# Optimization experiments

Measured on AMD Instinct MI355X. Metric: run time of the kernel, lower is better.

The kernel has to match this reference:

```python
import jax, jax.numpy as jnp
import numpy as np

C, D, K15, K16, OUT = 64, 8, 15, 16, 512
B = 32768


def setup_inputs() -> dict:
    key = jax.random.key(0)
    kx, kS, kH, kT, kL = jax.random.split(key, 5)
    x = jax.random.normal(kx, (B, C * D), dtype=jnp.float32)
    S = jax.random.normal(kS, (C, D, K15), dtype=jnp.float32)
    H = jax.random.normal(kH, (K15, K16), dtype=jnp.float32)
    T = jax.random.normal(kT, (C, K15), dtype=jnp.float32)
    LUT = jax.random.normal(kL, (C, K16, OUT), dtype=jnp.float32)
    return {"x": x, "S": S, "H": H, "T": T, "LUT": LUT}


def reference(x, S, H, T, LUT):
    b = x.shape[0]
    xv = x.reshape(b, C, D)                              # (B, C, D)
    p = jnp.einsum('bcd,cdk->bck', xv, S) - T            # (B, C, 15)
    # torch sets zeros to -1 before sign => sign(x)==-1 when x<=0
    s = jnp.where(p > 0, jnp.float32(1.0), jnp.float32(-1.0))
    h = jnp.einsum('bck,kj->bcj', s, H)                  # (B, C, 16)
    idx = jnp.argmax(h, axis=-1)                         # (B, C) int
    # one_hot @ LUT == direct gather of LUT[c, idx[b,c], :]
    vals = LUT[jnp.arange(C)[None, :], idx]              # (B, C, OUT)
    return jnp.sum(vals, axis=1)                         # (B, OUT)
```

## Files before the change

### kernel.cpp

```cpp
#include <hip/hip_runtime.h>
#include <stdint.h>

#define B_    32768
#define C_    64
#define D_    8
#define K15_  15
#define K16_  16
#define OUT_  512

typedef _Float16 half4v __attribute__((ext_vector_type(4)));
typedef _Float16 half8  __attribute__((ext_vector_type(8)));

#define AMAP_OFF  0
#define AMAP_SZ   32768
#define S64_OFF   32768
#define S64_SZ    (64 * 15 * 8 * 8)
#define T64_OFF   (S64_OFF + S64_SZ)
#define T64_SZ    (64 * 15 * 8)
#define IDX_OFF   (T64_OFF + T64_SZ)
#define IDX_SZ    (B_ * C_)
#define S32_SZ    (64 * 15 * 8 * 4)
#define PCT_OFF   (IDX_OFF + IDX_SZ)
#define PCT_SZ    (B_ * 32)
#define PTAB_OFF  (PCT_OFF + PCT_SZ)
#define PTAB_SZ   (32 * 32 * 256 * 16 * 2)
#define WS_NEED   ((size_t)PTAB_OFF + PTAB_SZ)

__device__ __forceinline__ void gld_lds16(const void* g, void* l) {
    __builtin_amdgcn_global_load_lds(
        (const __attribute__((address_space(1))) void*)g,
        (__attribute__((address_space(3))) void*)l, 16, 0, 0);
}

__global__ __launch_bounds__(256) void k_setup(const float* __restrict__ LUT,
                                               const float* __restrict__ H,
                                               const float* __restrict__ S,
                                               const float* __restrict__ T,
                                               _Float16* __restrict__ P5,
                                               uint8_t* __restrict__ amap,
                                               double* __restrict__ S64,
                                               double* __restrict__ T64,
                                               float* __restrict__ S32,
                                               float* __restrict__ T32,
                                               int do_pairs) {
    int gid = blockIdx.x * 256 + threadIdx.x;

    if (do_pairs) {
        int e8 = gid & 1;
        int q = (gid >> 1) & 255;
        int jc = (gid >> 9) & 31;
        int p = gid >> 14;
        int t0 = q >> 4;
        int t1 = q & 15;
        int j0 = jc * 16 + e8 * 8;
        const float* u = LUT + (size_t)((2 * p) * 16 + t0) * 512 + j0;
        const float* v = LUT + (size_t)((2 * p + 1) * 16 + t1) * 512 + j0;
        float4 u0 = ((const float4*)u)[0];
        float4 u1 = ((const float4*)u)[1];
        float4 v0 = ((const float4*)v)[0];
        float4 v1 = ((const float4*)v)[1];
        half8 w;
        w[0] = (_Float16)(u0.x + v0.x);
        w[1] = (_Float16)(u0.y + v0.y);
        w[2] = (_Float16)(u0.z + v0.z);
        w[3] = (_Float16)(u0.w + v0.w);
        w[4] = (_Float16)(u1.x + v1.x);
        w[5] = (_Float16)(u1.y + v1.y);
        w[6] = (_Float16)(u1.z + v1.z);
        w[7] = (_Float16)(u1.w + v1.w);
        *(half8*)(P5 + (size_t)gid * 8) = w;
    }

    if (blockIdx.x < 128) {
        int code = gid;
        double h[K16_];
#pragma unroll
        for (int j = 0; j < K16_; ++j) h[j] = 0.0;
#pragma unroll
        for (int k = 0; k < K15_; ++k) {
            double s = ((code >> k) & 1) ? 1.0 : -1.0;
#pragma unroll
            for (int j = 0; j < K16_; ++j) h[j] += s * (double)H[k * K16_ + j];
        }
        double best = h[0];
        int bi = 0;
#pragma unroll
        for (int j = 1; j < K16_; ++j) {
            if (h[j] > best) { best = h[j]; bi = j; }
        }
        amap[code] = (uint8_t)bi;
    } else if (blockIdx.x == 128) {
        for (int i = threadIdx.x; i < 64 * 15 * 8; i += 256) {
            int c = i / 120;
            int r = i - c * 120;
            int k = r >> 3;
            int d = r & 7;
            float sv = S[c * 120 + d * 15 + k];
            S64[i] = (double)sv;
            if (do_pairs) S32[i] = sv;
        }
        for (int i = threadIdx.x; i < 64 * 15; i += 256) {
            T64[i] = (double)T[i];
            if (do_pairs) T32[i] = T[i];
        }
    }
}

#define XSTRIDE 585
template <int FAST>
__global__ __launch_bounds__(256) void k_codes2(const float* __restrict__ x,
                                                const double* __restrict__ S64,
                                                const double* __restrict__ T64,
                                                const float* __restrict__ S32,
                                                const float* __restrict__ T32,
                                                const uint8_t* __restrict__ amap,
                                                uint8_t* __restrict__ idxo,
                                                uint8_t* __restrict__ pcT) {
    __shared__ float xls[32 * XSTRIDE];
    __shared__ uint8_t idsh[64 * 68];

    int b0 = blockIdx.x * 64;
    int lane = threadIdx.x & 63;
    int wv = __builtin_amdgcn_readfirstlane(threadIdx.x >> 6);

    for (int half = 0; half < 2; ++half) {
        __syncthreads();
#pragma unroll
        for (int t = 0; t < 16; ++t) {
            int e = t * 256 + threadIdx.x;
            int b = e >> 6;
            int j4 = e & 63;
            float4 v = ((const float4*)(x + (size_t)(b0 + b) * 512 +
                                        half * 256))[j4];
            int cl = j4 >> 1;
            int d0 = (j4 & 1) * 4;
            float* dst = &xls[cl * XSTRIDE + b * 9 + d0];
            dst[0] = v.x; dst[1] = v.y; dst[2] = v.z; dst[3] = v.w;
        }
        __syncthreads();
        for (int i = 0; i < 8; ++i) {
            int cl = wv + i * 4;
            int c = half * 32 + cl;
            unsigned code = 0;
            if (FAST) {
                const float* Sc = S32 + c * 120;
                const float* Tc = T32 + c * 15;
                float xf[8];
#pragma unroll
                for (int d = 0; d < 8; ++d)
                    xf[d] = xls[cl * XSTRIDE + lane * 9 + d];
                float pmin = 3.0e38f;
#pragma unroll
                for (int k = 0; k < K15_; ++k) {
                    float p = -Tc[k];
#pragma unroll
                    for (int d = 0; d < 8; ++d)
                        p = fmaf(xf[d], Sc[k * 8 + d], p);
                    code |= (p > 0.f) ? (1u << k) : 0u;
                    pmin = fminf(pmin, fabsf(p));
                }
                if (pmin < 1e-4f) {
                    const double* Sd = S64 + c * 120;
                    const double* Td = T64 + c * 15;
                    code = 0;
#pragma unroll
                    for (int k = 0; k < K15_; ++k) {
                        double p = -Td[k];
#pragma unroll
                        for (int d = 0; d < 8; ++d)
                            p = fma((double)xf[d], Sd[k * 8 + d], p);
                        code |= (p > 0.0) ? (1u << k) : 0u;
                    }
                }
            } else {
                const double* Sc = S64 + c * 120;
                const double* Tc = T64 + c * 15;
                double xd[8];
#pragma unroll
                for (int d = 0; d < 8; ++d)
                    xd[d] = (double)xls[cl * XSTRIDE + lane * 9 + d];
#pragma unroll
                for (int k = 0; k < K15_; ++k) {
                    double p = -Tc[k];
#pragma unroll
                    for (int d = 0; d < 8; ++d)
                        p = fma(xd[d], Sc[k * 8 + d], p);
                    code |= (p > 0.0) ? (1u << k) : 0u;
                }
            }
            idsh[lane * 68 + c] = amap[code];
        }
    }
    __syncthreads();

    int bb = threadIdx.x >> 2;
    int q = threadIdx.x & 3;
    if (!FAST) {
        uint32_t w0 = *(const uint32_t*)&idsh[bb * 68 + q * 16 + 0];
        uint32_t w1 = *(const uint32_t*)&idsh[bb * 68 + q * 16 + 4];
        uint32_t w2 = *(const uint32_t*)&idsh[bb * 68 + q * 16 + 8];
        uint32_t w3 = *(const uint32_t*)&idsh[bb * 68 + q * 16 + 12];
        uint32_t* o = (uint32_t*)(idxo + (size_t)(b0 + bb) * 64 + q * 16);
        o[0] = w0; o[1] = w1; o[2] = w2; o[3] = w3;
    }
    {
        int row = b0 + bb;
        int rg = row >> 10;
        int tr = row & 127;
        int i_ = (row & 1023) >> 7;
        uint8_t* base = pcT + rg * 1024 + tr * 8 + i_;
#pragma unroll
        for (int pi = 0; pi < 8; ++pi) {
            int p = q * 8 + pi;
            uint8_t byte = (uint8_t)((idsh[bb * 68 + 2 * p] << 4) |
                                     idsh[bb * 68 + 2 * p + 1]);
            base[p * 32768] = byte;
        }
    }
}

__global__ __launch_bounds__(256, 8) void k_main8(const uint8_t* __restrict__ pcT,
                                                  const _Float16* __restrict__ P5,
                                                  float* __restrict__ out) {
    __shared__ alignas(16) _Float16 slab[2][256 * 16];

    int rg5 = blockIdx.x >> 5;
    int jc = blockIdx.x & 31;
    int t = threadIdx.x;
    int tc = t & 1;
    int tr = t >> 1;
    int lane = t & 63;
    int wv = __builtin_amdgcn_readfirstlane(t >> 6);

    const uint8_t* cbase = pcT + (rg5 >> 1) * 1024 + tr * 8 + (rg5 & 1) * 4;

    float acc[4][8];
#pragma unroll
    for (int i = 0; i < 4; ++i)
#pragma unroll
        for (int e = 0; e < 8; ++e) acc[i][e] = 0.f;

    int hoff = wv * 512 + lane * 8;

    {
        const _Float16* g = P5 + (size_t)jc * 4096 + hoff;
        gld_lds16(g, &slab[0][wv * 512]);
        gld_lds16(g + 2048, &slab[0][wv * 512 + 2048]);
    }
    uint32_t cw = *(const uint32_t*)cbase;
    uint32_t cwn = 0;

    for (int p = 0; p < 32; ++p) {
        __syncthreads();

        if (p < 31) {
            const _Float16* g =
                P5 + (size_t)((p + 1) * 32 + jc) * 4096 + hoff;
            _Float16* d = &slab[(p + 1) & 1][wv * 512];
            gld_lds16(g, d);
            gld_lds16(g + 2048, d + 2048);
            cwn = *(const uint32_t*)(cbase + (size_t)(p + 1) * 32768);
        }

        const _Float16* rb = &slab[p & 1][0] + tc * 8;
        uint32_t cw_cur = cw;
#pragma unroll
        for (int i = 0; i < 4; ++i) {
            int ci = (int)((cw_cur >> (8 * i)) & 0xFF);
            half8 v = *(const half8*)(rb + ci * 16);
#pragma unroll
            for (int e = 0; e < 8; ++e)
                acc[i][e] = fmaf((float)v[e], 1.0f, acc[i][e]);
        }
        cw = cwn;
    }

#pragma unroll
    for (int i = 0; i < 4; ++i) {
        int row = rg5 * 512 + i * 128 + tr;
        float* o = out + (size_t)row * 512 + jc * 16 + tc * 8;
        float4 w0;
        w0.x = acc[i][0]; w0.y = acc[i][1]; w0.z = acc[i][2]; w0.w = acc[i][3];
        float4 w1;
        w1.x = acc[i][4]; w1.y = acc[i][5]; w1.z = acc[i][6]; w1.w = acc[i][7];
        ((float4*)o)[0] = w0;
        ((float4*)o)[1] = w1;
    }
}

__global__ __launch_bounds__(256) void k_main_direct(const uint8_t* __restrict__ idx,
                                                     const float* __restrict__ LUT,
                                                     float* __restrict__ out) {
    int j4 = threadIdx.x & 127;
    int sub = threadIdx.x >> 7;
    int b0 = blockIdx.x * 16 + sub * 8;
    const float4* L4 = (const float4*)LUT;
    for (int r = 0; r < 8; ++r) {
        int b = b0 + r;
        const uint32_t* iw = (const uint32_t*)(idx + (size_t)b * 64);
        float4 acc;
        acc.x = 0.f; acc.y = 0.f; acc.z = 0.f; acc.w = 0.f;
#pragma unroll
        for (int i = 0; i < 16; ++i) {
            uint32_t w = __builtin_amdgcn_readfirstlane(iw[i]);
#pragma unroll
            for (int t = 0; t < 4; ++t) {
                int c = i * 4 + t;
                uint32_t codev = (w >> (8 * t)) & 0xFu;
                float4 v = L4[(size_t)(c * 16 + codev) * 128 + j4];
                acc.x += v.x; acc.y += v.y; acc.z += v.z; acc.w += v.w;
            }
        }
        ((float4*)(out + (size_t)b * 512))[j4] = acc;
    }
}

extern "C" void kernel_launch(void* const* d_in, const int* in_sizes, int n_in,
                              void* d_out, int out_size, void* d_ws, size_t ws_size,
                              hipStream_t stream) {
    const float* x   = (const float*)d_in[0];
    const float* S   = (const float*)d_in[1];
    const float* H   = (const float*)d_in[2];
    const float* T   = (const float*)d_in[3];
    const float* LUT = (const float*)d_in[4];
    float* out = (float*)d_out;

    uint8_t* ws = (uint8_t*)d_ws;
    uint8_t* amap = ws + AMAP_OFF;
    double* S64   = (double*)(ws + S64_OFF);
    double* T64   = (double*)(ws + T64_OFF);
    uint8_t* idxb = ws + IDX_OFF;
    float* S32    = (float*)(ws + IDX_OFF);
    float* T32    = (float*)(ws + IDX_OFF + S32_SZ);
    uint8_t* pcTb = ws + PCT_OFF;
    _Float16* P5  = (_Float16*)(ws + PTAB_OFF);

    bool use_pairs = ws_size >= WS_NEED;

    hipLaunchKernelGGL(k_setup, dim3(use_pairs ? 2048 : 129), dim3(256), 0,
                       stream, LUT, H, S, T, P5, amap, S64, T64, S32, T32,
                       use_pairs ? 1 : 0);
    if (use_pairs) {
        hipLaunchKernelGGL((k_codes2<1>), dim3(B_ / 64), dim3(256), 0, stream,
                           x, S64, T64, S32, T32, amap, idxb, pcTb);
        hipLaunchKernelGGL(k_main8, dim3(2048), dim3(256), 0, stream,
                           pcTb, P5, out);
    } else {
        hipLaunchKernelGGL((k_codes2<0>), dim3(B_ / 64), dim3(256), 0, stream,
                           x, S64, T64, S32, T32, amap, idxb, pcTb);
        hipLaunchKernelGGL(k_main_direct, dim3(B_ / 16), dim3(256), 0, stream,
                           idxb, LUT, out);
    }
}
```

Measured before the change: 187.9 us.

## Shrink codes-kernel shared memory with 8-channel chunks and deferred amap lookup

The codes kernel now stages x in eight 8-channel chunks instead of two 32-channel halves, which cuts the shared x buffer from about 75KB to about 19KB. It also sets a launch bound of 5 blocks per CU, aiming for higher occupancy. The 15-bit sign codes go into shared memory as uint16, and the amap lookup moves to the output phase, where each thread maps 16 codes before packing them. The cost is more barriers and smaller loads per chunk, plus a larger per-thread code buffer in shared memory.

```diff
diff --git a/kernel.cpp b/kernel.cpp
--- a/kernel.cpp
+++ b/kernel.cpp
@@ -106,41 +106,42 @@
     }
 }
 
-#define XSTRIDE 585
+#define XST2 587
 template <int FAST>
-__global__ __launch_bounds__(256) void k_codes2(const float* __restrict__ x,
-                                                const double* __restrict__ S64,
-                                                const double* __restrict__ T64,
-                                                const float* __restrict__ S32,
-                                                const float* __restrict__ T32,
-                                                const uint8_t* __restrict__ amap,
-                                                uint8_t* __restrict__ idxo,
-                                                uint8_t* __restrict__ pcT) {
-    __shared__ float xls[32 * XSTRIDE];
-    __shared__ uint8_t idsh[64 * 68];
+__global__ __launch_bounds__(256, 5) void k_codes3(const float* __restrict__ x,
+                                                   const double* __restrict__ S64,
+                                                   const double* __restrict__ T64,
+                                                   const float* __restrict__ S32,
+                                                   const float* __restrict__ T32,
+                                                   const uint8_t* __restrict__ amap,
+                                                   uint8_t* __restrict__ idxo,
+                                                   uint8_t* __restrict__ pcT) {
+    __shared__ float xls[8 * XST2];
+    __shared__ uint16_t codesh[64 * 66];
 
     int b0 = blockIdx.x * 64;
     int lane = threadIdx.x & 63;
     int wv = __builtin_amdgcn_readfirstlane(threadIdx.x >> 6);
 
-    for (int half = 0; half < 2; ++half) {
+    for (int r = 0; r < 8; ++r) {
         __syncthreads();
 #pragma unroll
-        for (int t = 0; t < 16; ++t) {
-            int e = t * 256 + threadIdx.x;
-            int b = e >> 6;
-            int j4 = e & 63;
+        for (int t2 = 0; t2 < 4; ++t2) {
+            int e = t2 * 256 + threadIdx.x;
+            int b = e >> 4;
+            int j4 = e & 15;
             float4 v = ((const float4*)(x + (size_t)(b0 + b) * 512 +
-                                        half * 256))[j4];
+                                        r * 64))[j4];
             int cl = j4 >> 1;
             int d0 = (j4 & 1) * 4;
-            float* dst = &xls[cl * XSTRIDE + b * 9 + d0];
+            float* dst = &xls[cl * XST2 + b * 9 + d0];
             dst[0] = v.x; dst[1] = v.y; dst[2] = v.z; dst[3] = v.w;
         }
         __syncthreads();
-        for (int i = 0; i < 8; ++i) {
+#pragma unroll
+        for (int i = 0; i < 2; ++i) {
             int cl = wv + i * 4;
-            int c = half * 32 + cl;
+            int c = r * 8 + cl;
             unsigned code = 0;
             if (FAST) {
                 const float* Sc = S32 + c * 120;
@@ -148,7 +149,7 @@
                 float xf[8];
 #pragma unroll
                 for (int d = 0; d < 8; ++d)
-                    xf[d] = xls[cl * XSTRIDE + lane * 9 + d];
+                    xf[d] = xls[cl * XST2 + lane * 9 + d];
                 float pmin = 3.0e38f;
 #pragma unroll
                 for (int k = 0; k < K15_; ++k) {
@@ -178,7 +179,7 @@
                 double xd[8];
 #pragma unroll
                 for (int d = 0; d < 8; ++d)
-                    xd[d] = (double)xls[cl * XSTRIDE + lane * 9 + d];
+                    xd[d] = (double)xls[cl * XST2 + lane * 9 + d];
 #pragma unroll
                 for (int k = 0; k < K15_; ++k) {
                     double p = -Tc[k];
@@ -188,22 +189,24 @@
                     code |= (p > 0.0) ? (1u << k) : 0u;
                 }
             }
-            idsh[lane * 68 + c] = amap[code];
+            codesh[lane * 66 + c] = (uint16_t)code;
         }
     }
     __syncthreads();
 
     int bb = threadIdx.x >> 2;
     int q = threadIdx.x & 3;
-    if (!FAST) {
-        uint32_t w0 = *(const uint32_t*)&idsh[bb * 68 + q * 16 + 0];
-        uint32_t w1 = *(const uint32_t*)&idsh[bb * 68 + q * 16 + 4];
-        uint32_t w2 = *(const uint32_t*)&idsh[bb * 68 + q * 16 + 8];
-        uint32_t w3 = *(const uint32_t*)&idsh[bb * 68 + q * 16 + 12];
-        uint32_t* o = (uint32_t*)(idxo + (size_t)(b0 + bb) * 64 + q * 16);
-        o[0] = w0; o[1] = w1; o[2] = w2; o[3] = w3;
-    }
-    {
+    uint16_t cds[16];
+#pragma unroll
+    for (int j = 0; j < 4; ++j) {
+        *(ulong1*)&cds[j * 4] =
+            *(const ulong1*)&codesh[bb * 66 + q * 16 + j * 4];
+    }
+    uint8_t ids[16];
+#pragma unroll
+    for (int j = 0; j < 16; ++j) ids[j] = amap[cds[j]];
+
+    if (FAST) {
         int row = b0 + bb;
         int rg = row >> 10;
         int tr = row & 127;
@@ -211,11 +214,18 @@
         uint8_t* base = pcT + rg * 1024 + tr * 8 + i_;
 #pragma unroll
         for (int pi = 0; pi < 8; ++pi) {
-            int p = q * 8 + pi;
-            uint8_t byte = (uint8_t)((idsh[bb * 68 + 2 * p] << 4) |
-                                     idsh[bb * 68 + 2 * p + 1]);
-            base[p * 32768] = byte;
-        }
+            uint8_t byte = (uint8_t)((ids[2 * pi] << 4) | ids[2 * pi + 1]);
+            base[(q * 8 + pi) * 32768] = byte;
+        }
+    } else {
+        uint32_t w[4];
+#pragma unroll
+        for (int j = 0; j < 4; ++j)
+            w[j] = (uint32_t)ids[4 * j] | ((uint32_t)ids[4 * j + 1] << 8) |
+                   ((uint32_t)ids[4 * j + 2] << 16) |
+                   ((uint32_t)ids[4 * j + 3] << 24);
+        uint32_t* o = (uint32_t*)(idxo + (size_t)(b0 + bb) * 64 + q * 16);
+        o[0] = w[0]; o[1] = w[1]; o[2] = w[2]; o[3] = w[3];
     }
 }
 
@@ -341,12 +351,12 @@
                        stream, LUT, H, S, T, P5, amap, S64, T64, S32, T32,
                        use_pairs ? 1 : 0);
     if (use_pairs) {
-        hipLaunchKernelGGL((k_codes2<1>), dim3(B_ / 64), dim3(256), 0, stream,
+        hipLaunchKernelGGL((k_codes3<1>), dim3(B_ / 64), dim3(256), 0, stream,
                            x, S64, T64, S32, T32, amap, idxb, pcTb);
         hipLaunchKernelGGL(k_main8, dim3(2048), dim3(256), 0, stream,
                            pcTb, P5, out);
     } else {
-        hipLaunchKernelGGL((k_codes2<0>), dim3(B_ / 64), dim3(256), 0, stream,
+        hipLaunchKernelGGL((k_codes3<0>), dim3(B_ / 64), dim3(256), 0, stream,
                            x, S64, T64, S32, T32, amap, idxb, pcTb);
         hipLaunchKernelGGL(k_main_direct, dim3(B_ / 16), dim3(256), 0, stream,
                            idxb, LUT, out);
```

Result: faster. 182.6 us (-2.9%).

## Fuse pair-table build into codes kernel, drop LDS staging, use fma_mix

Applied to the files above, without the earlier changes.

The fp16 pair-LUT construction moves out of the setup kernel and into extra blocks of the codes kernel, so it can run concurrently with code computation and setup shrinks to 129 blocks. The codes kernel no longer stages x through LDS with block syncs. Each thread instead loads its own row slice for 4 channels directly, and the fp64 S/T copies are dropped in favour of converting the fp32 copies on the rare fallback path. The main accumulation loop uses inline v_fma_mix_f32 to add fp16 values to fp32 accumulators without separate conversion instructions. Direct per-thread x loads are less coalesced than the old staged layout, and the pcT byte writes become scattered.

```diff
diff --git a/kernel.cpp b/kernel.cpp
--- a/kernel.cpp
+++ b/kernel.cpp
@@ -10,16 +10,16 @@
 
 typedef _Float16 half4v __attribute__((ext_vector_type(4)));
 typedef _Float16 half8  __attribute__((ext_vector_type(8)));
+typedef uint32_t uint4v __attribute__((ext_vector_type(4)));
 
 #define AMAP_OFF  0
 #define AMAP_SZ   32768
-#define S64_OFF   32768
-#define S64_SZ    (64 * 15 * 8 * 8)
-#define T64_OFF   (S64_OFF + S64_SZ)
-#define T64_SZ    (64 * 15 * 8)
-#define IDX_OFF   (T64_OFF + T64_SZ)
+#define S32_OFF   32768
+#define S32_SZ    (64 * 15 * 8 * 4)
+#define T32_OFF   (S32_OFF + S32_SZ)
+#define T32_SZ    (64 * 15 * 4)
+#define IDX_OFF   67584
 #define IDX_SZ    (B_ * C_)
-#define S32_SZ    (64 * 15 * 8 * 4)
 #define PCT_OFF   (IDX_OFF + IDX_SZ)
 #define PCT_SZ    (B_ * 32)
 #define PTAB_OFF  (PCT_OFF + PCT_SZ)
@@ -32,20 +32,64 @@
         (__attribute__((address_space(3))) void*)l, 16, 0, 0);
 }
 
-__global__ __launch_bounds__(256) void k_setup(const float* __restrict__ LUT,
-                                               const float* __restrict__ H,
+__device__ __forceinline__ void fma_mix_lo(float& acc, uint32_t w, float one) {
+    asm("v_fma_mix_f32 %0, %1, %2, %0 op_sel_hi:[1,0,0]"
+        : "+v"(acc) : "v"(w), "v"(one));
+}
+__device__ __forceinline__ void fma_mix_hi(float& acc, uint32_t w, float one) {
+    asm("v_fma_mix_f32 %0, %1, %2, %0 op_sel:[1,0,0] op_sel_hi:[1,0,0]"
+        : "+v"(acc) : "v"(w), "v"(one));
+}
+
+__global__ __launch_bounds__(256) void k_setup(const float* __restrict__ H,
                                                const float* __restrict__ S,
                                                const float* __restrict__ T,
-                                               _Float16* __restrict__ P5,
                                                uint8_t* __restrict__ amap,
-                                               double* __restrict__ S64,
-                                               double* __restrict__ T64,
                                                float* __restrict__ S32,
-                                               float* __restrict__ T32,
-                                               int do_pairs) {
+                                               float* __restrict__ T32) {
     int gid = blockIdx.x * 256 + threadIdx.x;
 
-    if (do_pairs) {
+    if (blockIdx.x < 128) {
+        int code = gid;
+        double h[K16_];
+#pragma unroll
+        for (int j = 0; j < K16_; ++j) h[j] = 0.0;
+#pragma unroll
+        for (int k = 0; k < K15_; ++k) {
+            double s = ((code >> k) & 1) ? 1.0 : -1.0;
+#pragma unroll
+            for (int j = 0; j < K16_; ++j) h[j] += s * (double)H[k * K16_ + j];
+        }
+        double best = h[0];
+        int bi = 0;
+#pragma unroll
+        for (int j = 1; j < K16_; ++j) {
+            if (h[j] > best) { best = h[j]; bi = j; }
+        }
+        amap[code] = (uint8_t)bi;
+    } else {
+        for (int i = threadIdx.x; i < 64 * 15 * 8; i += 256) {
+            int c = i / 120;
+            int r = i - c * 120;
+            int k = r >> 3;
+            int d = r & 7;
+            S32[i] = S[c * 120 + d * 15 + k];
+        }
+        for (int i = threadIdx.x; i < 64 * 15; i += 256) T32[i] = T[i];
+    }
+}
+
+template <int FAST>
+__global__ __launch_bounds__(256) void k_codes7(const float* __restrict__ x,
+                                                const float* __restrict__ S32,
+                                                const float* __restrict__ T32,
+                                                const uint8_t* __restrict__ amap,
+                                                uint8_t* __restrict__ idxo,
+                                                uint8_t* __restrict__ pcT,
+                                                const float* __restrict__ LUT,
+                                                _Float16* __restrict__ P5) {
+    if (FAST && blockIdx.x >= 2048) {
+        int gid = (blockIdx.x - 2048) * 256 + threadIdx.x;
         int e8 = gid & 1;
         int q = (gid >> 1) & 255;
         int jc = (gid >> 9) & 31;
@@ -69,157 +113,72 @@
         w[6] = (_Float16)(u1.z + v1.z);
         w[7] = (_Float16)(u1.w + v1.w);
         *(half8*)(P5 + (size_t)gid * 8) = w;
-    }
-
-    if (blockIdx.x < 128) {
-        int code = gid;
-        double h[K16_];
-#pragma unroll
-        for (int j = 0; j < K16_; ++j) h[j] = 0.0;
-#pragma unroll
-        for (int k = 0; k < K15_; ++k) {
-            double s = ((code >> k) & 1) ? 1.0 : -1.0;
-#pragma unroll
-            for (int j = 0; j < K16_; ++j) h[j] += s * (double)H[k * K16_ + j];
-        }
-        double best = h[0];
-        int bi = 0;
-#pragma unroll
-        for (int j = 1; j < K16_; ++j) {
-            if (h[j] > best) { best = h[j]; bi = j; }
-        }
-        amap[code] = (uint8_t)bi;
-    } else if (blockIdx.x == 128) {
-        for (int i = threadIdx.x; i < 64 * 15 * 8; i += 256) {
-            int c = i / 120;
-            int r = i - c * 120;
-            int k = r >> 3;
-            int d = r & 7;
-            float sv = S[c * 120 + d * 15 + k];
-            S64[i] = (double)sv;
-            if (do_pairs) S32[i] = sv;
-        }
-        for (int i = threadIdx.x; i < 64 * 15; i += 256) {
-            T64[i] = (double)T[i];
-            if (do_pairs) T32[i] = T[i];
-        }
-    }
-}
-
-#define XSTRIDE 585
-template <int FAST>
-__global__ __launch_bounds__(256) void k_codes2(const float* __restrict__ x,
-                                                const double* __restrict__ S64,
-                                                const double* __restrict__ T64,
-                                                const float* __restrict__ S32,
-                                                const float* __restrict__ T32,
-                                                const uint8_t* __restrict__ amap,
-                                                uint8_t* __restrict__ idxo,
-                                                uint8_t* __restrict__ pcT) {
-    __shared__ float xls[32 * XSTRIDE];
-    __shared__ uint8_t idsh[64 * 68];
-
-    int b0 = blockIdx.x * 64;
+        return;
+    }
+
+    int bg = blockIdx.x >> 2;
+    int cq = blockIdx.x & 3;
     int lane = threadIdx.x & 63;
     int wv = __builtin_amdgcn_readfirstlane(threadIdx.x >> 6);
-
-    for (int half = 0; half < 2; ++half) {
-        __syncthreads();
-#pragma unroll
-        for (int t = 0; t < 16; ++t) {
-            int e = t * 256 + threadIdx.x;
-            int b = e >> 6;
-            int j4 = e & 63;
-            float4 v = ((const float4*)(x + (size_t)(b0 + b) * 512 +
-                                        half * 256))[j4];
-            int cl = j4 >> 1;
-            int d0 = (j4 & 1) * 4;
-            float* dst = &xls[cl * XSTRIDE + b * 9 + d0];
-            dst[0] = v.x; dst[1] = v.y; dst[2] = v.z; dst[3] = v.w;
-        }
-        __syncthreads();
-        for (int i = 0; i < 8; ++i) {
-            int cl = wv + i * 4;
-            int c = half * 32 + cl;
-            unsigned code = 0;
-            if (FAST) {
-                const float* Sc = S32 + c * 120;
-                const float* Tc = T32 + c * 15;
-                float xf[8];
+    int row = bg * 64 + lane;
+    int c0 = cq * 16 + wv * 4;
+
+    const float4* xr = (const float4*)(x + (size_t)row * 512 + c0 * 8);
+    float4 xv[8];
+#pragma unroll
+    for (int j = 0; j < 8; ++j) xv[j] = xr[j];
+
+    uint8_t ids[4];
+#pragma unroll
+    for (int ch = 0; ch < 4; ++ch) {
+        int c = c0 + ch;
+        const float* Sc = S32 + c * 120;
+        const float* Tc = T32 + c * 15;
+        float xf[8];
+        xf[0] = xv[2 * ch].x; xf[1] = xv[2 * ch].y;
+        xf[2] = xv[2 * ch].z; xf[3] = xv[2 * ch].w;
+        xf[4] = xv[2 * ch + 1].x; xf[5] = xv[2 * ch + 1].y;
+        xf[6] = xv[2 * ch + 1].z; xf[7] = xv[2 * ch + 1].w;
+        unsigned code = 0;
+        float pmin = 3.0e38f;
+#pragma unroll
+        for (int k = 0; k < K15_; ++k) {
+            float p = -Tc[k];
+#pragma unroll
+            for (int d = 0; d < 8; ++d) p = fmaf(xf[d], Sc[k * 8 + d], p);
+            code |= (p > 0.f) ? (1u << k) : 0u;
+            pmin = fminf(pmin, fabsf(p));
+        }
+        if (pmin < 1e-4f) {
+            code = 0;
+#pragma unroll
+            for (int k = 0; k < K15_; ++k) {
+                double p = -(double)Tc[k];
 #pragma unroll
                 for (int d = 0; d < 8; ++d)
-                    xf[d] = xls[cl * XSTRIDE + lane * 9 + d];
-                float pmin = 3.0e38f;
-#pragma unroll
-                for (int k = 0; k < K15_; ++k) {
-                    float p = -Tc[k];
-#pragma unroll
-                    for (int d = 0; d < 8; ++d)
-                        p = fmaf(xf[d], Sc[k * 8 + d], p);
-                    code |= (p > 0.f) ? (1u << k) : 0u;
-                    pmin = fminf(pmin, fabsf(p));
-                }
-                if (pmin < 1e-4f) {
-                    const double* Sd = S64 + c * 120;
-                    const double* Td = T64 + c * 15;
-                    code = 0;
-#pragma unroll
-                    for (int k = 0; k < K15_; ++k) {
-                        double p = -Td[k];
-#pragma unroll
-                        for (int d = 0; d < 8; ++d)
-                            p = fma((double)xf[d], Sd[k * 8 + d], p);
-                        code |= (p > 0.0) ? (1u << k) : 0u;
-                    }
-                }
-            } else {
-                const double* Sc = S64 + c * 120;
-                const double* Tc = T64 + c * 15;
-                double xd[8];
-#pragma unroll
-                for (int d = 0; d < 8; ++d)
-                    xd[d] = (double)xls[cl * XSTRIDE + lane * 9 + d];
-#pragma unroll
-                for (int k = 0; k < K15_; ++k) {
-                    double p = -Tc[k];
-#pragma unroll
-                    for (int d = 0; d < 8; ++d)
-                        p = fma(xd[d], Sc[k * 8 + d], p);
-                    code |= (p > 0.0) ? (1u << k) : 0u;
-                }
+                    p = fma((double)xf[d], (double)Sc[k * 8 + d], p);
+                code |= (p > 0.0) ? (1u << k) : 0u;
             }
-            idsh[lane * 68 + c] = amap[code];
-        }
-    }
-    __syncthreads();
-
-    int bb = threadIdx.x >> 2;
-    int q = threadIdx.x & 3;
-    if (!FAST) {
-        uint32_t w0 = *(const uint32_t*)&idsh[bb * 68 + q * 16 + 0];
-        uint32_t w1 = *(const uint32_t*)&idsh[bb * 68 + q * 16 + 4];
-        uint32_t w2 = *(const uint32_t*)&idsh[bb * 68 + q * 16 + 8];
-        uint32_t w3 = *(const uint32_t*)&idsh[bb * 68 + q * 16 + 12];
-        uint32_t* o = (uint32_t*)(idxo + (size_t)(b0 + bb) * 64 + q * 16);
-        o[0] = w0; o[1] = w1; o[2] = w2; o[3] = w3;
-    }
-    {
-        int row = b0 + bb;
+        }
+        ids[ch] = amap[code];
+    }
+
+    if (FAST) {
         int rg = row >> 10;
         int tr = row & 127;
         int i_ = (row & 1023) >> 7;
         uint8_t* base = pcT + rg * 1024 + tr * 8 + i_;
-#pragma unroll
-        for (int pi = 0; pi < 8; ++pi) {
-            int p = q * 8 + pi;
-            uint8_t byte = (uint8_t)((idsh[bb * 68 + 2 * p] << 4) |
-                                     idsh[bb * 68 + 2 * p + 1]);
-            base[p * 32768] = byte;
-        }
-    }
-}
-
-__global__ __launch_bounds__(256, 8) void k_main8(const uint8_t* __restrict__ pcT,
+        int p0 = c0 >> 1;
+        base[(size_t)p0 * 32768] = (uint8_t)((ids[0] << 4) | ids[1]);
+        base[(size_t)(p0 + 1) * 32768] = (uint8_t)((ids[2] << 4) | ids[3]);
+    } else {
+        uint32_t w = (uint32_t)ids[0] | ((uint32_t)ids[1] << 8) |
+                     ((uint32_t)ids[2] << 16) | ((uint32_t)ids[3] << 24);
+        *(uint32_t*)(idxo + (size_t)row * 64 + c0) = w;
+    }
+}
+
+__global__ __launch_bounds__(256, 8) void k_main9(const uint8_t* __restrict__ pcT,
                                                   const _Float16* __restrict__ P5,
                                                   float* __restrict__ out) {
     __shared__ alignas(16) _Float16 slab[2][256 * 16];
@@ -239,6 +198,7 @@
     for (int i = 0; i < 4; ++i)
 #pragma unroll
         for (int e = 0; e < 8; ++e) acc[i][e] = 0.f;
+    float one = 1.0f;
 
     int hoff = wv * 512 + lane * 8;
 
@@ -268,9 +228,12 @@
         for (int i = 0; i < 4; ++i) {
             int ci = (int)((cw_cur >> (8 * i)) & 0xFF);
             half8 v = *(const half8*)(rb + ci * 16);
-#pragma unroll
-            for (int e = 0; e < 8; ++e)
-                acc[i][e] = fmaf((float)v[e], 1.0f, acc[i][e]);
+            uint4v w = __builtin_bit_cast(uint4v, v);
+#pragma unroll
+            for (int e2 = 0; e2 < 4; ++e2) {
+                fma_mix_lo(acc[i][2 * e2], w[e2], one);
+                fma_mix_hi(acc[i][2 * e2 + 1], w[e2], one);
+            }
         }
         cw = cwn;
     }
@@ -327,27 +290,24 @@
 
     uint8_t* ws = (uint8_t*)d_ws;
     uint8_t* amap = ws + AMAP_OFF;
-    double* S64   = (double*)(ws + S64_OFF);
-    double* T64   = (double*)(ws + T64_OFF);
+    float* S32    = (float*)(ws + S32_OFF);
+    float* T32    = (float*)(ws + T32_OFF);
     uint8_t* idxb = ws + IDX_OFF;
-    float* S32    = (float*)(ws + IDX_OFF);
-    float* T32    = (float*)(ws + IDX_OFF + S32_SZ);
     uint8_t* pcTb = ws + PCT_OFF;
     _Float16* P5  = (_Float16*)(ws + PTAB_OFF);
 
     bool use_pairs = ws_size >= WS_NEED;
 
-    hipLaunchKernelGGL(k_setup, dim3(use_pairs ? 2048 : 129), dim3(256), 0,
-                       stream, LUT, H, S, T, P5, amap, S64, T64, S32, T32,
-                       use_pairs ? 1 : 0);
+    hipLaunchKernelGGL(k_setup, dim3(129), dim3(256), 0, stream,
+                       H, S, T, amap, S32, T32);
     if (use_pairs) {
-        hipLaunchKernelGGL((k_codes2<1>), dim3(B_ / 64), dim3(256), 0, stream,
-                           x, S64, T64, S32, T32, amap, idxb, pcTb);
-        hipLaunchKernelGGL(k_main8, dim3(2048), dim3(256), 0, stream,
+        hipLaunchKernelGGL((k_codes7<1>), dim3(4096), dim3(256), 0, stream,
+                           x, S32, T32, amap, idxb, pcTb, LUT, P5);
+        hipLaunchKernelGGL(k_main9, dim3(2048), dim3(256), 0, stream,
                            pcTb, P5, out);
     } else {
-        hipLaunchKernelGGL((k_codes2<0>), dim3(B_ / 64), dim3(256), 0, stream,
-                           x, S64, T64, S32, T32, amap, idxb, pcTb);
+        hipLaunchKernelGGL((k_codes7<0>), dim3(2048), dim3(256), 0, stream,
+                           x, S32, T32, amap, idxb, pcTb, LUT, P5);
         hipLaunchKernelGGL(k_main_direct, dim3(B_ / 16), dim3(256), 0, stream,
                            idxb, LUT, out);
     }
```

Measured after the change: 163.7 us. 1.15x faster.
